# Optimization experiments

Hardware: AMD Instinct MI355X
Metric: run time of the kernel (lower is better)

## Reference

```python
import jax, jax.numpy as jnp
import numpy as np

BATCH, SEQ_LEN, INPUT_DIM, HIDDEN, OUT_DIM = 4096, 2048, 5, 64, 1
DT = 0.1


def setup_inputs() -> dict:
    key = jax.random.key(0)
    ks = jax.random.split(key, 8)
    return {
        "x": jax.random.normal(ks[0], (BATCH, SEQ_LEN, INPUT_DIM), dtype=jnp.float32),
        # torch.rand(hidden)*0.5 + 0.1  -> uniform in [0.1, 0.6)
        "time_constants": jax.random.uniform(ks[1], (HIDDEN,), dtype=jnp.float32) * 0.5 + 0.1,
        "W_ih_w": jax.random.normal(ks[2], (HIDDEN, INPUT_DIM), dtype=jnp.float32) * (1.0 / np.sqrt(INPUT_DIM)),
        "W_ih_b": jax.random.normal(ks[3], (HIDDEN,), dtype=jnp.float32) * 0.02,
        "W_hh_w": jax.random.normal(ks[4], (HIDDEN, HIDDEN), dtype=jnp.float32) * (1.0 / np.sqrt(HIDDEN)),
        "W_hh_b": jax.random.normal(ks[5], (HIDDEN,), dtype=jnp.float32) * 0.02,
        "out_w": jax.random.normal(ks[6], (OUT_DIM, HIDDEN), dtype=jnp.float32) * (1.0 / np.sqrt(HIDDEN)),
        "out_b": jax.random.normal(ks[7], (OUT_DIM,), dtype=jnp.float32) * 0.02,
    }


def reference(x, time_constants, W_ih_w, W_ih_b, W_hh_w, W_hh_b, out_w, out_b):
    # x: [B, T, D_in]. Liquid-time-constant RNN: sequential scan over T.
    batch = x.shape[0]
    hidden = time_constants.shape[0]
    inv_tau = 1.0 / jnp.abs(time_constants)  # [H], hoisted out of the loop

    def step(h, x_t):
        # x_t: [B, D_in], h: [B, H]
        input_current = x_t @ W_ih_w.T + W_ih_b            # [B, H]
        recurrent_current = jnp.tanh(h) @ W_hh_w.T + W_hh_b  # [B, H]
        dhdt = -h * inv_tau + input_current + recurrent_current
        return h + DT * dhdt, None

    h0 = jnp.zeros((batch, hidden), dtype=x.dtype)
    xs = jnp.swapaxes(x, 0, 1)  # [T, B, D_in]
    h_final, _ = jax.lax.scan(step, h0, xs)
    return jnp.tanh(h_final) @ out_w.T + out_b  # [B, out_dim]
```

## Files before the change

kernel.cpp:

```cpp
#include <hip/hip_runtime.h>
#include <hip/hip_bf16.h>
#include <stdint.h>

#define SEQ     2048
#define DIN     5
#define HID     64
#define DTC     0.1f
#define BTILE   16
#define NWAVE   4

typedef __attribute__((ext_vector_type(8))) __bf16  bf16x8;
typedef __attribute__((ext_vector_type(8))) short   short8;
typedef __attribute__((ext_vector_type(4))) float   f32x4;
typedef __attribute__((ext_vector_type(4))) int     i32x4;
typedef unsigned long long u64;

__device__ __forceinline__ unsigned short f2bf(float f) {
    unsigned int u = __builtin_bit_cast(unsigned int, f);
    return (unsigned short)((u + 0x7FFFu + ((u >> 16) & 1u)) >> 16);
}

__device__ __forceinline__ float fast_tanh(float x) {
    float e = __expf(2.0f * x);
    return 1.0f - 2.0f * __builtin_amdgcn_rcpf(e + 1.0f);
}

__device__ __forceinline__ unsigned int cvt_pk_bf16(float lo, float hi) {
    unsigned int r;
    asm("v_cvt_pk_bf16_f32 %0, %1, %2" : "=v"(r) : "v"(lo), "v"(hi));
    return r;
}

__global__ __launch_bounds__(256) void ltc_kernel(
    const float* __restrict__ x,
    const float* __restrict__ tau,
    const float* __restrict__ Wih,
    const float* __restrict__ bih,
    const float* __restrict__ Whh,
    const float* __restrict__ bhh,
    const float* __restrict__ outw,
    const float* __restrict__ outb,
    float* __restrict__ out)
{
    const int tid  = threadIdx.x;
    const int wave = tid >> 6;
    const int lane = tid & 63;
    const int lg   = lane >> 4;
    const int ln   = lane & 15;
    const int b0   = blockIdx.x * BTILE;

    __shared__ __align__(16) unsigned short sbuf[2][1024];
    __shared__ float redbuf[NWAVE][4][BTILE];

    const int jbase = 16 * wave + 4 * lg;
    const int arow  = 16 * wave + ln;

    float a[4], ow[4];
#pragma unroll
    for (int r = 0; r < 4; ++r) {
        a[r]  = 1.0f - DTC / fabsf(tau[jbase + r]);
        ow[r] = outw[jbase + r];
    }

    short8 s0 = {0,0,0,0,0,0,0,0}, s1 = {0,0,0,0,0,0,0,0}, s2 = {0,0,0,0,0,0,0,0};
#pragma unroll
    for (int q = 0; q < 8; ++q) {
        s0[q] = (short)f2bf(DTC * Whh[arow * HID + lg * 8 + q]);
        s1[q] = (short)f2bf(DTC * Whh[arow * HID + 32 + lg * 8 + q]);
    }
    if (lg == 0) {
#pragma unroll
        for (int d = 0; d < DIN; ++d) s2[d] = (short)f2bf(DTC * Wih[arow * DIN + d]);
        s2[5] = (short)f2bf(DTC * (bih[arow] + bhh[arow]));
    }
    const bf16x8 Ahh0 = __builtin_bit_cast(bf16x8, s0);
    const bf16x8 Ahh1 = __builtin_bit_cast(bf16x8, s1);
    const bf16x8 Aix  = __builtin_bit_cast(bf16x8, s2);

    const int wbyte = ((jbase >= 32) ? 1024 : 0) + (((jbase & 31) >> 3) * 256)
                    + ln * 16 + (((jbase >> 2) & 1) * 8);
    char* const wp0 = (char*)sbuf[0] + wbyte;
    char* const wp1 = (char*)sbuf[1] + wbyte;
    const char* const rp0 = (const char*)sbuf[0] + lane * 16;
    const char* const rp1 = (const char*)sbuf[1] + lane * 16;

    ((u64*)sbuf[1])[tid] = 0ULL;

    const unsigned int lmask = (lg == 0) ? 0xFFFFFFFFu : 0u;

    const float* xb = x + (size_t)(b0 + ln) * (SEQ * DIN);
    float eA0 = xb[0], eA1 = xb[1], eA2 = xb[2], eA3 = xb[3], eA4 = xb[4];
    float oA0 = xb[5], oA1 = xb[6], oA2 = xb[7], oA3 = xb[8], oA4 = xb[9];
    const float* xnext = xb + 2 * DIN;

    f32x4 h = {0.f, 0.f, 0.f, 0.f};

#define STEP(PAR, P0, P1, P2, P3, P4, PF, XOFF)                                    \
    {                                                                              \
        __syncthreads();                                                           \
        const char* rb = (PAR) ? rp0 : rp1;                \
        i32x4 r0 = *(const i32x4*)(rb);                                            \
        i32x4 r1 = *(const i32x4*)(rb + 1024);                                     \
        unsigned int bu0 = cvt_pk_bf16(P0, P1) & lmask;                            \
        unsigned int bu1 = cvt_pk_bf16(P2, P3) & lmask;                            \
        unsigned int bu2 = cvt_pk_bf16(P4, 1.0f) & lmask;                          \
        i32x4 bx = { (int)bu0, (int)bu1, (int)bu2, 0 };                            \
        if (PF) { P0 = xnext[(XOFF)+0]; P1 = xnext[(XOFF)+1]; P2 = xnext[(XOFF)+2];\
                  P3 = xnext[(XOFF)+3]; P4 = xnext[(XOFF)+4]; }                    \
        f32x4 c;                                                                   \
        c[0] = a[0]*h[0]; c[1] = a[1]*h[1]; c[2] = a[2]*h[2]; c[3] = a[3]*h[3];    \
        c = __builtin_amdgcn_mfma_f32_16x16x32_bf16(Aix,  __builtin_bit_cast(bf16x8, bx), c, 0, 0, 0); \
        c = __builtin_amdgcn_mfma_f32_16x16x32_bf16(Ahh0, __builtin_bit_cast(bf16x8, r0), c, 0, 0, 0); \
        c = __builtin_amdgcn_mfma_f32_16x16x32_bf16(Ahh1, __builtin_bit_cast(bf16x8, r1), c, 0, 0, 0); \
        h = c;                                                                     \
        float t0 = fast_tanh(h[0]), t1 = fast_tanh(h[1]);                          \
        float t2 = fast_tanh(h[2]), t3 = fast_tanh(h[3]);                          \
        u64 w01 = ((u64)cvt_pk_bf16(t2, t3) << 32) | (u64)cvt_pk_bf16(t0, t1);     \
        *(u64*)((PAR) ? wp1 : wp0) = w01;                                          \
    }

    for (int t = 0; t < SEQ - 2; t += 2) {
        STEP(0, eA0, eA1, eA2, eA3, eA4, true, 0)
        STEP(1, oA0, oA1, oA2, oA3, oA4, true, DIN)
        xnext += 2 * DIN;
    }
    STEP(0, eA0, eA1, eA2, eA3, eA4, false, 0)
    STEP(1, oA0, oA1, oA2, oA3, oA4, false, 0)
#undef STEP

    float part = fast_tanh(h[0]) * ow[0] + fast_tanh(h[1]) * ow[1]
               + fast_tanh(h[2]) * ow[2] + fast_tanh(h[3]) * ow[3];
    redbuf[wave][lg][ln] = part;
    __syncthreads();
    if (tid < BTILE) {
        float s = outb[0];
#pragma unroll
        for (int w = 0; w < NWAVE; ++w)
#pragma unroll
            for (int g = 0; g < 4; ++g) s += redbuf[w][g][tid];
        out[b0 + tid] = s;
    }
}

extern "C" void kernel_launch(void* const* d_in, const int* in_sizes, int n_in,
                              void* d_out, int out_size, void* d_ws, size_t ws_size,
                              hipStream_t stream) {
    const float* x    = (const float*)d_in[0];
    const float* tau  = (const float*)d_in[1];
    const float* Wih  = (const float*)d_in[2];
    const float* bih  = (const float*)d_in[3];
    const float* Whh  = (const float*)d_in[4];
    const float* bhh  = (const float*)d_in[5];
    const float* outw = (const float*)d_in[6];
    const float* outb = (const float*)d_in[7];
    float* out = (float*)d_out;

    const int batch = in_sizes[0] / (SEQ * DIN);
    ltc_kernel<<<batch / BTILE, NWAVE * 64, 0, stream>>>(x, tau, Wih, bih, Whh, bhh, outw, outb, out);
}
```

Baseline: 523.9 us.

## Process four independent 16-column batch tiles per block to interleave recurrences

Each block now handles 64 batch columns as four independent 16-wide groups, with their MFMA chains and tanh computations interleaved inside each time step. The goal is instruction-level parallelism that hides MFMA and transcendental latency, and one barrier per step spread over four times the work. The trade-off is that the grid shrinks to a quarter as many blocks, so far fewer CUs are busy on a latency-bound sequential scan. Register and LDS use per block also grow. The lane mask on the input operand is dropped, relying on the zero-padded weight fragment for lanes outside the first group.

```diff
diff --git a/kernel.cpp b/kernel.cpp
--- a/kernel.cpp
+++ b/kernel.cpp
@@ -2,17 +2,19 @@
 #include <hip/hip_bf16.h>
 #include <stdint.h>
 
-#define SEQ     2048
-#define DIN     5
-#define HID     64
-#define DTC     0.1f
-#define BTILE   16
-#define NWAVE   4
+#define SEQ   2048
+#define DIN   5
+#define HID   64
+#define DTC   0.1f
+#define NW    4
+#define GT    4
+#define COLS  (16*GT)
 
 typedef __attribute__((ext_vector_type(8))) __bf16  bf16x8;
 typedef __attribute__((ext_vector_type(8))) short   short8;
 typedef __attribute__((ext_vector_type(4))) float   f32x4;
 typedef __attribute__((ext_vector_type(4))) int     i32x4;
+typedef __attribute__((ext_vector_type(2))) int     i32x2;
 typedef unsigned long long u64;
 
 __device__ __forceinline__ unsigned short f2bf(float f) {
@@ -47,10 +49,10 @@
     const int lane = tid & 63;
     const int lg   = lane >> 4;
     const int ln   = lane & 15;
-    const int b0   = blockIdx.x * BTILE;
+    const int b0   = blockIdx.x * COLS;
 
-    __shared__ __align__(16) unsigned short sbuf[2][1024];
-    __shared__ float redbuf[NWAVE][4][BTILE];
+    __shared__ __align__(16) unsigned short sbuf[2][GT][1024];
+    __shared__ float redbuf[GT][NW][4][16];
 
     const int jbase = 16 * wave + 4 * lg;
     const int arow  = 16 * wave + ln;
@@ -79,65 +81,88 @@
 
     const int wbyte = ((jbase >= 32) ? 1024 : 0) + (((jbase & 31) >> 3) * 256)
                     + ln * 16 + (((jbase >> 2) & 1) * 8);
-    char* const wp0 = (char*)sbuf[0] + wbyte;
-    char* const wp1 = (char*)sbuf[1] + wbyte;
-    const char* const rp0 = (const char*)sbuf[0] + lane * 16;
-    const char* const rp1 = (const char*)sbuf[1] + lane * 16;
 
-    ((u64*)sbuf[1])[tid] = 0ULL;
+#pragma unroll
+    for (int i = 0; i < GT; ++i) ((u64*)sbuf[1])[tid + 256 * i] = 0ULL;
 
-    const unsigned int lmask = (lg == 0) ? 0xFFFFFFFFu : 0u;
+    const float* xp[GT];
+    float ex[GT][DIN], ox[GT][DIN];
+#pragma unroll
+    for (int g = 0; g < GT; ++g) {
+        xp[g] = x + (size_t)(b0 + 16 * g + ln) * (SEQ * DIN);
+#pragma unroll
+        for (int d = 0; d < DIN; ++d) { ex[g][d] = xp[g][d]; ox[g][d] = xp[g][DIN + d]; }
+    }
 
-    const float* xb = x + (size_t)(b0 + ln) * (SEQ * DIN);
-    float eA0 = xb[0], eA1 = xb[1], eA2 = xb[2], eA3 = xb[3], eA4 = xb[4];
-    float oA0 = xb[5], oA1 = xb[6], oA2 = xb[7], oA3 = xb[8], oA4 = xb[9];
-    const float* xnext = xb + 2 * DIN;
+    f32x4 h[GT];
+#pragma unroll
+    for (int g = 0; g < GT; ++g) { h[g][0]=0.f; h[g][1]=0.f; h[g][2]=0.f; h[g][3]=0.f; }
 
-    f32x4 h = {0.f, 0.f, 0.f, 0.f};
+    int xoff = 2 * DIN;
 
-#define STEP(PAR, P0, P1, P2, P3, P4, PF, XOFF)                                    \
-    {                                                                              \
-        __syncthreads();                                                           \
-        const char* rb = (PAR) ? rp0 : rp1;                \
-        i32x4 r0 = *(const i32x4*)(rb);                                            \
-        i32x4 r1 = *(const i32x4*)(rb + 1024);                                     \
-        unsigned int bu0 = cvt_pk_bf16(P0, P1) & lmask;                            \
-        unsigned int bu1 = cvt_pk_bf16(P2, P3) & lmask;                            \
-        unsigned int bu2 = cvt_pk_bf16(P4, 1.0f) & lmask;                          \
-        i32x4 bx = { (int)bu0, (int)bu1, (int)bu2, 0 };                            \
-        if (PF) { P0 = xnext[(XOFF)+0]; P1 = xnext[(XOFF)+1]; P2 = xnext[(XOFF)+2];\
-                  P3 = xnext[(XOFF)+3]; P4 = xnext[(XOFF)+4]; }                    \
-        f32x4 c;                                                                   \
-        c[0] = a[0]*h[0]; c[1] = a[1]*h[1]; c[2] = a[2]*h[2]; c[3] = a[3]*h[3];    \
-        c = __builtin_amdgcn_mfma_f32_16x16x32_bf16(Aix,  __builtin_bit_cast(bf16x8, bx), c, 0, 0, 0); \
-        c = __builtin_amdgcn_mfma_f32_16x16x32_bf16(Ahh0, __builtin_bit_cast(bf16x8, r0), c, 0, 0, 0); \
-        c = __builtin_amdgcn_mfma_f32_16x16x32_bf16(Ahh1, __builtin_bit_cast(bf16x8, r1), c, 0, 0, 0); \
-        h = c;                                                                     \
-        float t0 = fast_tanh(h[0]), t1 = fast_tanh(h[1]);                          \
-        float t2 = fast_tanh(h[2]), t3 = fast_tanh(h[3]);                          \
-        u64 w01 = ((u64)cvt_pk_bf16(t2, t3) << 32) | (u64)cvt_pk_bf16(t0, t1);     \
-        *(u64*)((PAR) ? wp1 : wp0) = w01;                                          \
+#define STEP(PAR, PX, PF, XADD)                                                      \
+    {                                                                                \
+        __syncthreads();                                                             \
+        i32x4 r0[GT], r1[GT];                                                        \
+        _Pragma("unroll")                                                            \
+        for (int g = 0; g < GT; ++g) {                                               \
+            const char* rb = (const char*)sbuf + ((PAR) ^ 1) * 8192 + g * 2048 + lane * 16; \
+            r0[g] = *(const i32x4*)rb;                                               \
+            r1[g] = *(const i32x4*)(rb + 1024);                                      \
+        }                                                                            \
+        i32x4 bx[GT];                                                                \
+        _Pragma("unroll")                                                            \
+        for (int g = 0; g < GT; ++g) {                                               \
+            bx[g][0] = (int)cvt_pk_bf16(PX[g][0], PX[g][1]);                         \
+            bx[g][1] = (int)cvt_pk_bf16(PX[g][2], PX[g][3]);                         \
+            bx[g][2] = (int)cvt_pk_bf16(PX[g][4], 1.0f);                             \
+            bx[g][3] = 0;                                                            \
+        }                                                                            \
+        if (PF) {                                                                    \
+            _Pragma("unroll")                                                        \
+            for (int g = 0; g < GT; ++g)                                             \
+                _Pragma("unroll")                                                    \
+                for (int d = 0; d < DIN; ++d) PX[g][d] = xp[g][xoff + (XADD) + d];   \
+        }                                                                            \
+        _Pragma("unroll")                                                            \
+        for (int g = 0; g < GT; ++g) {                                               \
+            f32x4 c;                                                                 \
+            c[0] = a[0]*h[g][0]; c[1] = a[1]*h[g][1];                                \
+            c[2] = a[2]*h[g][2]; c[3] = a[3]*h[g][3];                                \
+            c = __builtin_amdgcn_mfma_f32_16x16x32_bf16(Aix,  __builtin_bit_cast(bf16x8, bx[g]), c, 0, 0, 0); \
+            c = __builtin_amdgcn_mfma_f32_16x16x32_bf16(Ahh0, __builtin_bit_cast(bf16x8, r0[g]), c, 0, 0, 0); \
+            c = __builtin_amdgcn_mfma_f32_16x16x32_bf16(Ahh1, __builtin_bit_cast(bf16x8, r1[g]), c, 0, 0, 0); \
+            h[g] = c;                                                                \
+            float t0 = fast_tanh(c[0]), t1 = fast_tanh(c[1]);                        \
+            float t2 = fast_tanh(c[2]), t3 = fast_tanh(c[3]);                        \
+            i32x2 w; w[0] = (int)cvt_pk_bf16(t0, t1); w[1] = (int)cvt_pk_bf16(t2, t3); \
+            *(i32x2*)((char*)sbuf + (PAR) * 8192 + g * 2048 + wbyte) = w;            \
+        }                                                                            \
     }
 
     for (int t = 0; t < SEQ - 2; t += 2) {
-        STEP(0, eA0, eA1, eA2, eA3, eA4, true, 0)
-        STEP(1, oA0, oA1, oA2, oA3, oA4, true, DIN)
-        xnext += 2 * DIN;
+        STEP(0, ex, true, 0)
+        STEP(1, ox, true, DIN)
+        xoff += 2 * DIN;
     }
-    STEP(0, eA0, eA1, eA2, eA3, eA4, false, 0)
-    STEP(1, oA0, oA1, oA2, oA3, oA4, false, 0)
+    STEP(0, ex, false, 0)
+    STEP(1, ox, false, 0)
 #undef STEP
 
-    float part = fast_tanh(h[0]) * ow[0] + fast_tanh(h[1]) * ow[1]
-               + fast_tanh(h[2]) * ow[2] + fast_tanh(h[3]) * ow[3];
-    redbuf[wave][lg][ln] = part;
+#pragma unroll
+    for (int g = 0; g < GT; ++g) {
+        float part = fast_tanh(h[g][0]) * ow[0] + fast_tanh(h[g][1]) * ow[1]
+                   + fast_tanh(h[g][2]) * ow[2] + fast_tanh(h[g][3]) * ow[3];
+        redbuf[g][wave][lg][ln] = part;
+    }
     __syncthreads();
-    if (tid < BTILE) {
+    if (tid < COLS) {
+        const int g = tid >> 4, c = tid & 15;
         float s = outb[0];
 #pragma unroll
-        for (int w = 0; w < NWAVE; ++w)
+        for (int w = 0; w < NW; ++w)
 #pragma unroll
-            for (int g = 0; g < 4; ++g) s += redbuf[w][g][tid];
+            for (int l = 0; l < 4; ++l) s += redbuf[g][w][l][c];
         out[b0 + tid] = s;
     }
 }
@@ -156,5 +181,5 @@
     float* out = (float*)d_out;
 
     const int batch = in_sizes[0] / (SEQ * DIN);
-    ltc_kernel<<<batch / BTILE, NWAVE * 64, 0, stream>>>(x, tau, Wih, bih, Whh, bhh, outw, outb, out);
+    ltc_kernel<<<batch / COLS, NW * 64, 0, stream>>>(x, tau, Wih, bih, Whh, bhh, outw, outb, out);
 }
```

After: 1.986 ms. 3.79x slower.

## Pack two independent batch groups per 512-thread block and drop input lane mask

Applied to the files above, without the earlier changes.

Each block now runs two independent 16-row batch groups: 8 waves with separate LDS double buffers, sharing one block-wide barrier per step. The grid shrinks to half as many blocks. The intent is to hide the per-step MFMA, tanh and LDS latency of one group behind the other on the same CU. It also removes the lane mask on the packed input operand, which is safe because the A-operand rows for the other lane groups are zero. The risks are that only half as many blocks exist to spread across CUs, and that the barrier now couples two unrelated recurrences.

```diff
diff --git a/kernel.cpp b/kernel.cpp
--- a/kernel.cpp
+++ b/kernel.cpp
@@ -2,17 +2,18 @@
 #include <hip/hip_bf16.h>
 #include <stdint.h>
 
-#define SEQ     2048
-#define DIN     5
-#define HID     64
-#define DTC     0.1f
-#define BTILE   16
-#define NWAVE   4
+#define SEQ   2048
+#define DIN   5
+#define HID   64
+#define DTC   0.1f
+#define NGRP  2
+#define NW4   4
 
 typedef __attribute__((ext_vector_type(8))) __bf16  bf16x8;
 typedef __attribute__((ext_vector_type(8))) short   short8;
 typedef __attribute__((ext_vector_type(4))) float   f32x4;
 typedef __attribute__((ext_vector_type(4))) int     i32x4;
+typedef __attribute__((ext_vector_type(2))) int     i32x2;
 typedef unsigned long long u64;
 
 __device__ __forceinline__ unsigned short f2bf(float f) {
@@ -31,7 +32,7 @@
     return r;
 }
 
-__global__ __launch_bounds__(256) void ltc_kernel(
+__global__ __launch_bounds__(512) void ltc_kernel(
     const float* __restrict__ x,
     const float* __restrict__ tau,
     const float* __restrict__ Wih,
@@ -45,15 +46,17 @@
     const int tid  = threadIdx.x;
     const int wave = tid >> 6;
     const int lane = tid & 63;
+    const int g2   = wave >> 2;
+    const int w4   = wave & 3;
     const int lg   = lane >> 4;
     const int ln   = lane & 15;
-    const int b0   = blockIdx.x * BTILE;
+    const int b0   = blockIdx.x * (16 * NGRP) + g2 * 16;
 
-    __shared__ __align__(16) unsigned short sbuf[2][1024];
-    __shared__ float redbuf[NWAVE][4][BTILE];
+    __shared__ __align__(16) unsigned short sbuf[NGRP][2][1024];
+    __shared__ float redbuf[NGRP][NW4][4][16];
 
-    const int jbase = 16 * wave + 4 * lg;
-    const int arow  = 16 * wave + ln;
+    const int jbase = 16 * w4 + 4 * lg;
+    const int arow  = 16 * w4 + ln;
 
     float a[4], ow[4];
 #pragma unroll
@@ -79,66 +82,69 @@
 
     const int wbyte = ((jbase >= 32) ? 1024 : 0) + (((jbase & 31) >> 3) * 256)
                     + ln * 16 + (((jbase >> 2) & 1) * 8);
-    char* const wp0 = (char*)sbuf[0] + wbyte;
-    char* const wp1 = (char*)sbuf[1] + wbyte;
-    const char* const rp0 = (const char*)sbuf[0] + lane * 16;
-    const char* const rp1 = (const char*)sbuf[1] + lane * 16;
+    char* const wp0 = (char*)&sbuf[g2][0][0] + wbyte;
+    char* const wp1 = (char*)&sbuf[g2][1][0] + wbyte;
+    const char* const rp0 = (const char*)&sbuf[g2][0][0] + lane * 16;
+    const char* const rp1 = (const char*)&sbuf[g2][1][0] + lane * 16;
 
-    ((u64*)sbuf[1])[tid] = 0ULL;
-
-    const unsigned int lmask = (lg == 0) ? 0xFFFFFFFFu : 0u;
+    ((u64*)&sbuf[g2][1][0])[w4 * 64 + lane] = 0ULL;
 
     const float* xb = x + (size_t)(b0 + ln) * (SEQ * DIN);
-    float eA0 = xb[0], eA1 = xb[1], eA2 = xb[2], eA3 = xb[3], eA4 = xb[4];
-    float oA0 = xb[5], oA1 = xb[6], oA2 = xb[7], oA3 = xb[8], oA4 = xb[9];
+    float ex[DIN], ox[DIN];
+#pragma unroll
+    for (int d = 0; d < DIN; ++d) { ex[d] = xb[d]; ox[d] = xb[DIN + d]; }
     const float* xnext = xb + 2 * DIN;
 
     f32x4 h = {0.f, 0.f, 0.f, 0.f};
 
-#define STEP(PAR, P0, P1, P2, P3, P4, PF, XOFF)                                    \
+#define STEP(PAR, PX, PF, XADD)                                                    \
     {                                                                              \
         __syncthreads();                                                           \
         const char* rb = (PAR) ? rp0 : rp1;                \
         i32x4 r0 = *(const i32x4*)(rb);                                            \
         i32x4 r1 = *(const i32x4*)(rb + 1024);                                     \
-        unsigned int bu0 = cvt_pk_bf16(P0, P1) & lmask;                            \
-        unsigned int bu1 = cvt_pk_bf16(P2, P3) & lmask;                            \
-        unsigned int bu2 = cvt_pk_bf16(P4, 1.0f) & lmask;                          \
-        i32x4 bx = { (int)bu0, (int)bu1, (int)bu2, 0 };                            \
-        if (PF) { P0 = xnext[(XOFF)+0]; P1 = xnext[(XOFF)+1]; P2 = xnext[(XOFF)+2];\
-                  P3 = xnext[(XOFF)+3]; P4 = xnext[(XOFF)+4]; }                    \
+        i32x4 bx;                                                                  \
+        bx[0] = (int)cvt_pk_bf16(PX[0], PX[1]);                                    \
+        bx[1] = (int)cvt_pk_bf16(PX[2], PX[3]);                                    \
+        bx[2] = (int)cvt_pk_bf16(PX[4], 1.0f);                                     \
+        bx[3] = 0;                                                                 \
+        if (PF) {                                                                  \
+            _Pragma("unroll")                                                      \
+            for (int d = 0; d < DIN; ++d) PX[d] = xnext[(XADD) + d];               \
+        }                                                                          \
         f32x4 c;                                                                   \
         c[0] = a[0]*h[0]; c[1] = a[1]*h[1]; c[2] = a[2]*h[2]; c[3] = a[3]*h[3];    \
         c = __builtin_amdgcn_mfma_f32_16x16x32_bf16(Aix,  __builtin_bit_cast(bf16x8, bx), c, 0, 0, 0); \
         c = __builtin_amdgcn_mfma_f32_16x16x32_bf16(Ahh0, __builtin_bit_cast(bf16x8, r0), c, 0, 0, 0); \
         c = __builtin_amdgcn_mfma_f32_16x16x32_bf16(Ahh1, __builtin_bit_cast(bf16x8, r1), c, 0, 0, 0); \
         h = c;                                                                     \
-        float t0 = fast_tanh(h[0]), t1 = fast_tanh(h[1]);                          \
-        float t2 = fast_tanh(h[2]), t3 = fast_tanh(h[3]);                          \
-        u64 w01 = ((u64)cvt_pk_bf16(t2, t3) << 32) | (u64)cvt_pk_bf16(t0, t1);     \
-        *(u64*)((PAR) ? wp1 : wp0) = w01;                                          \
+        float t0 = fast_tanh(c[0]), t1 = fast_tanh(c[1]);                          \
+        float t2 = fast_tanh(c[2]), t3 = fast_tanh(c[3]);                          \
+        i32x2 w; w[0] = (int)cvt_pk_bf16(t0, t1); w[1] = (int)cvt_pk_bf16(t2, t3); \
+        *(i32x2*)((PAR) ? wp1 : wp0) = w;                                          \
     }
 
     for (int t = 0; t < SEQ - 2; t += 2) {
-        STEP(0, eA0, eA1, eA2, eA3, eA4, true, 0)
-        STEP(1, oA0, oA1, oA2, oA3, oA4, true, DIN)
+        STEP(0, ex, true, 0)
+        STEP(1, ox, true, DIN)
         xnext += 2 * DIN;
     }
-    STEP(0, eA0, eA1, eA2, eA3, eA4, false, 0)
-    STEP(1, oA0, oA1, oA2, oA3, oA4, false, 0)
+    STEP(0, ex, false, 0)
+    STEP(1, ox, false, 0)
 #undef STEP
 
     float part = fast_tanh(h[0]) * ow[0] + fast_tanh(h[1]) * ow[1]
                + fast_tanh(h[2]) * ow[2] + fast_tanh(h[3]) * ow[3];
-    redbuf[wave][lg][ln] = part;
+    redbuf[g2][w4][lg][ln] = part;
     __syncthreads();
-    if (tid < BTILE) {
+    if (tid < 16 * NGRP) {
+        const int g = tid >> 4, cix = tid & 15;
         float s = outb[0];
 #pragma unroll
-        for (int w = 0; w < NWAVE; ++w)
+        for (int w = 0; w < NW4; ++w)
 #pragma unroll
-            for (int g = 0; g < 4; ++g) s += redbuf[w][g][tid];
-        out[b0 + tid] = s;
+            for (int l = 0; l < 4; ++l) s += redbuf[g][w][l][cix];
+        out[blockIdx.x * (16 * NGRP) + tid] = s;
     }
 }
 
@@ -156,5 +162,5 @@
     float* out = (float*)d_out;
 
     const int batch = in_sizes[0] / (SEQ * DIN);
-    ltc_kernel<<<batch / BTILE, NWAVE * 64, 0, stream>>>(x, tau, Wih, bih, Whh, bhh, outw, outb, out);
+    ltc_kernel<<<batch / (16 * NGRP), 512, 0, stream>>>(x, tau, Wih, bih, Whh, bhh, outw, outb, out);
 }
```

After: 889.6 us. 1.7x slower.

## Double-buffer x in 8-step vector chunks and use an LDS-only barrier

Applied to the files above, without the earlier changes.

Each 8-timestep chunk of x is now loaded as ten float4 vectors into register buffers. The next chunk's loads are issued one super-step ahead in a double-buffered pattern. The per-step __syncthreads is replaced by an inline barrier that waits only on lgkmcnt, so in-flight global loads of x no longer stall every step's barrier. The lane mask on the input B operand is dropped, relying on the zero Aix rows for lanes outside group 0. In exchange, register pressure rises from the 80 buffered floats, and correctness depends on hand-coded waitcnt semantics.

```diff
diff --git a/kernel.cpp b/kernel.cpp
--- a/kernel.cpp
+++ b/kernel.cpp
@@ -2,17 +2,18 @@
 #include <hip/hip_bf16.h>
 #include <stdint.h>
 
-#define SEQ     2048
-#define DIN     5
-#define HID     64
-#define DTC     0.1f
-#define BTILE   16
-#define NWAVE   4
+#define SEQ   2048
+#define DIN   5
+#define HID   64
+#define DTC   0.1f
+#define BTILE 16
+#define NWAVE 4
 
 typedef __attribute__((ext_vector_type(8))) __bf16  bf16x8;
 typedef __attribute__((ext_vector_type(8))) short   short8;
 typedef __attribute__((ext_vector_type(4))) float   f32x4;
 typedef __attribute__((ext_vector_type(4))) int     i32x4;
+typedef __attribute__((ext_vector_type(2))) int     i32x2;
 typedef unsigned long long u64;
 
 __device__ __forceinline__ unsigned short f2bf(float f) {
@@ -86,47 +87,59 @@
 
     ((u64*)sbuf[1])[tid] = 0ULL;
 
-    const unsigned int lmask = (lg == 0) ? 0xFFFFFFFFu : 0u;
-
     const float* xb = x + (size_t)(b0 + ln) * (SEQ * DIN);
-    float eA0 = xb[0], eA1 = xb[1], eA2 = xb[2], eA3 = xb[3], eA4 = xb[4];
-    float oA0 = xb[5], oA1 = xb[6], oA2 = xb[7], oA3 = xb[8], oA4 = xb[9];
-    const float* xnext = xb + 2 * DIN;
+    f32x4 bufA[10], bufB[10];
+#pragma unroll
+    for (int i = 0; i < 10; ++i) bufA[i] = *(const f32x4*)(xb + 4 * i);
 
     f32x4 h = {0.f, 0.f, 0.f, 0.f};
 
-#define STEP(PAR, P0, P1, P2, P3, P4, PF, XOFF)                                    \
+#define SBAR() asm volatile("s_waitcnt lgkmcnt(0)\n\ts_barrier" ::: "memory")
+
+#define BODY(PAR, X0, X1, X2, X3, X4)                                              \
     {                                                                              \
-        __syncthreads();                                                           \
         const char* rb = (PAR) ? rp0 : rp1;                \
         i32x4 r0 = *(const i32x4*)(rb);                                            \
         i32x4 r1 = *(const i32x4*)(rb + 1024);                                     \
-        unsigned int bu0 = cvt_pk_bf16(P0, P1) & lmask;                            \
-        unsigned int bu1 = cvt_pk_bf16(P2, P3) & lmask;                            \
-        unsigned int bu2 = cvt_pk_bf16(P4, 1.0f) & lmask;                          \
-        i32x4 bx = { (int)bu0, (int)bu1, (int)bu2, 0 };                            \
-        if (PF) { P0 = xnext[(XOFF)+0]; P1 = xnext[(XOFF)+1]; P2 = xnext[(XOFF)+2];\
-                  P3 = xnext[(XOFF)+3]; P4 = xnext[(XOFF)+4]; }                    \
+        i32x4 bx;                                                                  \
+        bx[0] = (int)cvt_pk_bf16(X0, X1);                                          \
+        bx[1] = (int)cvt_pk_bf16(X2, X3);                                          \
+        bx[2] = (int)cvt_pk_bf16(X4, 1.0f);                                        \
+        bx[3] = 0;                                                                 \
         f32x4 c;                                                                   \
         c[0] = a[0]*h[0]; c[1] = a[1]*h[1]; c[2] = a[2]*h[2]; c[3] = a[3]*h[3];    \
         c = __builtin_amdgcn_mfma_f32_16x16x32_bf16(Aix,  __builtin_bit_cast(bf16x8, bx), c, 0, 0, 0); \
         c = __builtin_amdgcn_mfma_f32_16x16x32_bf16(Ahh0, __builtin_bit_cast(bf16x8, r0), c, 0, 0, 0); \
         c = __builtin_amdgcn_mfma_f32_16x16x32_bf16(Ahh1, __builtin_bit_cast(bf16x8, r1), c, 0, 0, 0); \
         h = c;                                                                     \
-        float t0 = fast_tanh(h[0]), t1 = fast_tanh(h[1]);                          \
-        float t2 = fast_tanh(h[2]), t3 = fast_tanh(h[3]);                          \
-        u64 w01 = ((u64)cvt_pk_bf16(t2, t3) << 32) | (u64)cvt_pk_bf16(t0, t1);     \
-        *(u64*)((PAR) ? wp1 : wp0) = w01;                                          \
+        float t0 = fast_tanh(c[0]), t1 = fast_tanh(c[1]);                          \
+        float t2 = fast_tanh(c[2]), t3 = fast_tanh(c[3]);                          \
+        i32x2 w; w[0] = (int)cvt_pk_bf16(t0, t1); w[1] = (int)cvt_pk_bf16(t2, t3); \
+        *(i32x2*)((PAR) ? wp1 : wp0) = w;                                          \
     }
 
-    for (int t = 0; t < SEQ - 2; t += 2) {
-        STEP(0, eA0, eA1, eA2, eA3, eA4, true, 0)
-        STEP(1, oA0, oA1, oA2, oA3, oA4, true, DIN)
-        xnext += 2 * DIN;
+#define SUPER(BUF, DO_LOAD, LBUF, LOFF)                                            \
+    SBAR();                                                                        \
+    if (DO_LOAD) {                                                                 \
+        _Pragma("unroll")                                                          \
+        for (int i = 0; i < 10; ++i) LBUF[i] = *(const f32x4*)(xb + (LOFF) + 4*i); \
+    }                                                                              \
+    BODY(0, BUF[0][0], BUF[0][1], BUF[0][2], BUF[0][3], BUF[1][0])                 \
+    SBAR(); BODY(1, BUF[1][1], BUF[1][2], BUF[1][3], BUF[2][0], BUF[2][1])         \
+    SBAR(); BODY(0, BUF[2][2], BUF[2][3], BUF[3][0], BUF[3][1], BUF[3][2])         \
+    SBAR(); BODY(1, BUF[3][3], BUF[4][0], BUF[4][1], BUF[4][2], BUF[4][3])         \
+    SBAR(); BODY(0, BUF[5][0], BUF[5][1], BUF[5][2], BUF[5][3], BUF[6][0])         \
+    SBAR(); BODY(1, BUF[6][1], BUF[6][2], BUF[6][3], BUF[7][0], BUF[7][1])         \
+    SBAR(); BODY(0, BUF[7][2], BUF[7][3], BUF[8][0], BUF[8][1], BUF[8][2])         \
+    SBAR(); BODY(1, BUF[8][3], BUF[9][0], BUF[9][1], BUF[9][2], BUF[9][3])
+
+    for (int it = 0; it < SEQ / 16; ++it) {
+        SUPER(bufA, true,            bufB, (it * 16 + 8)  * DIN)
+        SUPER(bufB, it != SEQ/16 - 1, bufA, (it * 16 + 16) * DIN)
     }
-    STEP(0, eA0, eA1, eA2, eA3, eA4, false, 0)
-    STEP(1, oA0, oA1, oA2, oA3, oA4, false, 0)
-#undef STEP
+#undef SUPER
+#undef BODY
+#undef SBAR
 
     float part = fast_tanh(h[0]) * ow[0] + fast_tanh(h[1]) * ow[1]
                + fast_tanh(h[2]) * ow[2] + fast_tanh(h[3]) * ow[3];
```

Measured after the change: 531.7 us. About the same (+1.5%).
